# Kernel optimization log

Measured on AMD Instinct MI355X. Metric: run time of the kernel, lower is better.

Reference implementation:

```python
import jax, jax.numpy as jnp
import numpy as np

DIN = 1024
DOUT = 1024
NUM_HEAD = 16
HEAD_DIM = DIN // NUM_HEAD  # 64
SEQ = 2048
BS = 4


def setup_inputs() -> dict:
    key = jax.random.key(0)
    ks = jax.random.split(key, 9)
    s_in = 1.0 / np.sqrt(DIN)
    s_out = 1.0 / np.sqrt(DOUT)
    return {
        "x": jax.random.normal(ks[0], (BS, SEQ, DIN), dtype=jnp.float32),
        "Wq": jax.random.normal(ks[1], (DIN, DOUT), dtype=jnp.float32) * s_in,
        "bq": jax.random.normal(ks[2], (DOUT,), dtype=jnp.float32) * s_in,
        "Wk": jax.random.normal(ks[3], (DIN, DOUT), dtype=jnp.float32) * s_in,
        "bk": jax.random.normal(ks[4], (DOUT,), dtype=jnp.float32) * s_in,
        "Wv": jax.random.normal(ks[5], (DIN, DOUT), dtype=jnp.float32) * s_in,
        "bv": jax.random.normal(ks[6], (DOUT,), dtype=jnp.float32) * s_in,
        "Wo": jax.random.normal(ks[7], (DOUT, DOUT), dtype=jnp.float32) * s_out,
        "bo": jax.random.normal(ks[8], (DOUT,), dtype=jnp.float32) * s_out,
    }


def reference(x, Wq, bq, Wk, bk, Wv, bv, Wo, bo):
    bs, n, _ = x.shape
    # projections -> [bs, n, H, hd] -> [bs, H, n, hd]
    def split_heads(t):
        return t.reshape(bs, n, NUM_HEAD, HEAD_DIM).transpose(0, 2, 1, 3)

    q = split_heads(x @ Wq + bq)
    k = split_heads(x @ Wk + bk)
    v = split_heads(x @ Wv + bv)

    # full [bs, H, n, n] scores, causal mask, scaled softmax
    scores = jnp.einsum("bhqd,bhkd->bhqk", q, k)
    causal = jnp.tril(jnp.ones((n, n), dtype=bool))
    scores = jnp.where(causal, scores, -jnp.inf)
    att = jax.nn.softmax(scores / np.sqrt(HEAD_DIM), axis=-1)

    ctx = jnp.einsum("bhqk,bhkd->bhqd", att, v)
    ctx = ctx.transpose(0, 2, 1, 3).reshape(bs, n, DOUT)
    return ctx @ Wo + bo
```

## Files before the change

kernel.cpp:

```cpp
#include <hip/hip_runtime.h>
#include <hip/hip_bf16.h>
#include <stdint.h>

#define DIN   1024
#define DOUT  1024
#define NHEAD 16
#define HDIM  64
#define SEQL  2048
#define BSZ   4
#define MTOT  (BSZ*SEQL)
#define KDIM  1024

typedef __bf16 bf16x8 __attribute__((ext_vector_type(8)));
typedef float  f32x4  __attribute__((ext_vector_type(4)));

__device__ __forceinline__ f32x4 mfma16(bf16x8 a, bf16x8 b, f32x4 c) {
    return __builtin_amdgcn_mfma_f32_16x16x32_bf16(a, b, c, 0, 0, 0);
}

__device__ __forceinline__ void gl_lds16(const void* gsrc, void* ldst) {
    __builtin_amdgcn_global_load_lds(
        (const __attribute__((address_space(1))) uint32_t*)gsrc,
        (__attribute__((address_space(3))) uint32_t*)ldst, 16, 0, 0);
}

#if __has_builtin(__builtin_amdgcn_exp2f)
__device__ __forceinline__ float fexp2(float x) { return __builtin_amdgcn_exp2f(x); }
#else
__device__ __forceinline__ float fexp2(float x) { return exp2f(x); }
#endif

__device__ __forceinline__ unsigned int cvtpk(float lo, float hi) {
    unsigned int r;
    asm("v_cvt_pk_bf16_f32 %0, %1, %2" : "=v"(r) : "v"(lo), "v"(hi));
    return r;
}

__device__ __forceinline__ unsigned short f2bf(float f) {
    union { __hip_bfloat16 h; unsigned short u; } cv;
    cv.h = __float2bfloat16(f);
    return cv.u;
}

__global__ void cvt_bf16(const float4* __restrict__ in, ushort4* __restrict__ out, int n4) {
    int idx = blockIdx.x * blockDim.x + threadIdx.x;
    int stride = gridDim.x * blockDim.x;
    for (int i = idx; i < n4; i += stride) {
        float4 v = in[i];
        ushort4 o;
        o.x = f2bf(v.x); o.y = f2bf(v.y); o.z = f2bf(v.z); o.w = f2bf(v.w);
        out[i] = o;
    }
}

__global__ void transpose_cvt3(const float* __restrict__ W0, const float* __restrict__ W1,
                               const float* __restrict__ W2, __hip_bfloat16* __restrict__ Wt3) {
    __shared__ __hip_bfloat16 t[32][33];
    const int tx = threadIdx.x, ty = threadIdx.y;
    const int bx = blockIdx.x, by = blockIdx.y, z = blockIdx.z;
    const float* W = (z == 0) ? W0 : (z == 1) ? W1 : W2;
    __hip_bfloat16* Wt = Wt3 + (size_t)z * DOUT * DIN;
#pragma unroll
    for (int r = 0; r < 4; ++r)
        t[ty + 8*r][tx] = __float2bfloat16(W[(size_t)(by*32 + ty + 8*r) * DOUT + bx*32 + tx]);
    __syncthreads();
#pragma unroll
    for (int r = 0; r < 4; ++r)
        Wt[(size_t)(bx*32 + ty + 8*r) * DIN + by*32 + tx] = t[tx][ty + 8*r];
}

__global__ void transpose_cvt(const float* __restrict__ W, __hip_bfloat16* __restrict__ Wt) {
    __shared__ __hip_bfloat16 t[32][33];
    const int tx = threadIdx.x, ty = threadIdx.y;
    const int bx = blockIdx.x, by = blockIdx.y;
#pragma unroll
    for (int r = 0; r < 4; ++r)
        t[ty + 8*r][tx] = __float2bfloat16(W[(size_t)(by*32 + ty + 8*r) * DOUT + bx*32 + tx]);
    __syncthreads();
#pragma unroll
    for (int r = 0; r < 4; ++r)
        Wt[(size_t)(bx*32 + ty + 8*r) * DIN + by*32 + tx] = t[tx][ty + 8*r];
}

template <int EPI>
__global__ __launch_bounds__(256)
void gemm_mfma(const __hip_bfloat16* __restrict__ A,
               const __hip_bfloat16* __restrict__ Bt,
               const float* __restrict__ b0, const float* __restrict__ b1,
               void* __restrict__ o0, void* __restrict__ o1,
               float scale)
{
    __shared__ alignas(16) __hip_bfloat16 As[2][4][128][8];
    __shared__ alignas(16) __hip_bfloat16 Bs[2][4][128][8];

    const int tid  = threadIdx.x;
    const int w    = tid >> 6;
    const int lane = tid & 63;
    const int g    = lane >> 4;
    const int r    = lane & 15;
    const int wr   = w >> 1, wc = w & 1;

    const int row0 = blockIdx.y * 128;
    const int col0 = blockIdx.x * 128;

    f32x4 acc[4][4];
#pragma unroll
    for (int m = 0; m < 4; ++m)
#pragma unroll
        for (int n = 0; n < 4; ++n) acc[m][n] = (f32x4)0.0f;

    auto stage = [&](int buf, int kt) {
        const __hip_bfloat16* ga = A  + (size_t)(row0 + lane) * KDIM + kt*32 + 8*w;
        const __hip_bfloat16* gb = Bt + (size_t)(col0 + lane) * KDIM + kt*32 + 8*w;
        gl_lds16(ga,            &As[buf][w][0][0]);
        gl_lds16(ga + 64*KDIM,  &As[buf][w][64][0]);
        gl_lds16(gb,            &Bs[buf][w][0][0]);
        gl_lds16(gb + 64*KDIM,  &Bs[buf][w][64][0]);
    };

    stage(0, 0);
    __syncthreads();

    const int NKT = KDIM / 32;
    for (int kt = 0; kt < NKT; ++kt) {
        const int cur = kt & 1;
        if (kt + 1 < NKT) stage(cur ^ 1, kt + 1);

        bf16x8 af[4], bfr[4];
#pragma unroll
        for (int m = 0; m < 4; ++m)
            af[m] = *reinterpret_cast<const bf16x8*>(&As[cur][g][64*wr + 16*m + r][0]);
#pragma unroll
        for (int n = 0; n < 4; ++n)
            bfr[n] = *reinterpret_cast<const bf16x8*>(&Bs[cur][g][64*wc + 16*n + r][0]);

#pragma unroll
        for (int m = 0; m < 4; ++m)
#pragma unroll
            for (int n = 0; n < 4; ++n) {
                if (EPI == 1) acc[m][n] = mfma16(af[m], bfr[n], acc[m][n]);
                else          acc[m][n] = mfma16(bfr[n], af[m], acc[m][n]);
            }

        __syncthreads();
    }

    if (EPI == 0) {
        const int slab = col0 >> 10;
        const float* bp = (slab == 0) ? b0 : b1;
        __hip_bfloat16* op = (__hip_bfloat16*)((slab == 0) ? o0 : o1);
        const float sc = (slab == 0) ? scale : 1.0f;
#pragma unroll
        for (int m = 0; m < 4; ++m) {
            const int rowg = row0 + 64*wr + 16*m + r;
            const int bb = rowg >> 11, sq = rowg & (SEQL-1);
#pragma unroll
            for (int n = 0; n < 4; ++n) {
                const int c2 = (col0 & 1023) + 64*wc + 16*n + 4*g;
                const int hh = c2 >> 6, dd = c2 & (HDIM-1);
                const float4 bv4 = *reinterpret_cast<const float4*>(&bp[c2]);
                ushort4 ov;
                ov.x = f2bf((acc[m][n][0] + bv4.x) * sc);
                ov.y = f2bf((acc[m][n][1] + bv4.y) * sc);
                ov.z = f2bf((acc[m][n][2] + bv4.z) * sc);
                ov.w = f2bf((acc[m][n][3] + bv4.w) * sc);
                *reinterpret_cast<ushort4*>(
                    &op[(((size_t)(bb*NHEAD + hh) * SEQL + sq) << 6) + dd]) = ov;
            }
        }
    } else if (EPI == 1) {
#pragma unroll
        for (int n = 0; n < 4; ++n) {
            const int colg = col0 + 64*wc + 16*n + r;
            const int hhd = colg >> 6, dd = colg & (HDIM-1);
            const int n2 = dd >> 4, r2 = dd & 15;
            const float bv_ = b0[colg];
#pragma unroll
            for (int m = 0; m < 4; ++m) {
                const int rowg0 = row0 + 64*wr + 16*m + 4*g;
                const int bb = rowg0 >> 11, sq0 = rowg0 & (SEQL-1);
                const int kb = sq0 >> 6;
                const int hh2 = (sq0 >> 5) & 1;
                const int g2 = (sq0 >> 3) & 3;
                const int e0 = sq0 & 7;
                ushort4 ov;
                ov.x = f2bf(acc[m][n][0] + bv_);
                ov.y = f2bf(acc[m][n][1] + bv_);
                ov.z = f2bf(acc[m][n][2] + bv_);
                ov.w = f2bf(acc[m][n][3] + bv_);
                const size_t off = (size_t)(bb*NHEAD + hhd) * (SEQL*HDIM)
                    + ((((size_t)kb*4 + n2)*2 + hh2)*64 + 16*g2 + r2)*8 + e0;
                *reinterpret_cast<ushort4*>(&((__hip_bfloat16*)o0)[off]) = ov;
            }
        }
    } else {
#pragma unroll
        for (int m = 0; m < 4; ++m) {
            const int rowg = row0 + 64*wr + 16*m + r;
#pragma unroll
            for (int n = 0; n < 4; ++n) {
                const int colg0 = col0 + 64*wc + 16*n + 4*g;
                const float4 bv4 = *reinterpret_cast<const float4*>(&b0[colg0]);
                float4 ov;
                ov.x = acc[m][n][0] + bv4.x;
                ov.y = acc[m][n][1] + bv4.y;
                ov.z = acc[m][n][2] + bv4.z;
                ov.w = acc[m][n][3] + bv4.w;
                *reinterpret_cast<float4*>(&((float*)o0)[(size_t)rowg * DOUT + colg0]) = ov;
            }
        }
    }
}

__global__ __launch_bounds__(256)
void attn_fwd(const __hip_bfloat16* __restrict__ Q,
              const __hip_bfloat16* __restrict__ K,
              const __hip_bfloat16* __restrict__ Vff,
              __hip_bfloat16* __restrict__ ctx)
{
    __shared__ alignas(16) __hip_bfloat16 Ps[4][16][64];
    __shared__ alignas(16) f32x4 Om[2][64][16];
    __shared__ float Ml[2][64][9];

    const int tid  = threadIdx.x;
    const int w    = tid >> 6;
    const int lane = tid & 63;
    const int g    = lane >> 4;
    const int r    = lane & 15;
    const int swz  = (r & 7) << 3;
    const int pp   = w >> 1;
    const int half = w & 1;

    const int bh = blockIdx.x;
    const int b  = bh >> 4, h = bh & 15;

    const __hip_bfloat16* Qh = Q   + (size_t)bh * SEQL * HDIM;
    const __hip_bfloat16* Kh = K   + (size_t)bh * SEQL * HDIM;
    const __hip_bfloat16* Vh = Vff + (size_t)bh * SEQL * HDIM;

    const int sp = blockIdx.y * 2 + pp;

#pragma unroll 1
    for (int ti = 0; ti < 2; ++ti) {
        const int strip = ti ? (31 - sp) : sp;
        const int qb = strip * 64;

        bf16x8 qf[4][2];
#pragma unroll
        for (int m = 0; m < 4; ++m)
#pragma unroll
            for (int hh = 0; hh < 2; ++hh)
                qf[m][hh] = *reinterpret_cast<const bf16x8*>(
                    Qh + (size_t)(qb + 16*m + r) * HDIM + 32*hh + 8*g);

        f32x4 o[4][4];
        float mrow[4], lrow[4];
#pragma unroll
        for (int m = 0; m < 4; ++m) {
#pragma unroll
            for (int n = 0; n < 4; ++n) o[m][n] = (f32x4)0.0f;
            mrow[m] = -1e30f; lrow[m] = 0.0f;
        }

        const int nst = strip + 1;
        const int ns2 = (nst + 1) >> 1;
        const int k0  = half ? ns2 : 0;
        const int k1  = half ? nst : ns2;

        const __hip_bfloat16* kp01 = Kh + (size_t)(k0*64 + r) * HDIM + 8*g;
        const __hip_bfloat16* kp23 = kp01 + 32*HDIM;
        const __hip_bfloat16* vpA = Vh + (size_t)k0 * 4096 + lane * 8;
        const __hip_bfloat16* vpB = vpA + 2048;

#pragma unroll 1
        for (int kt = k0; kt < k1; ++kt) {
            const int key0 = kt * 64;

            bf16x8 kf[4][2], vf[4][2];
#pragma unroll
            for (int hh = 0; hh < 2; ++hh) {
                kf[0][hh] = *reinterpret_cast<const bf16x8*>(kp01 + hh*32);
                kf[1][hh] = *reinterpret_cast<const bf16x8*>(kp01 + 16*HDIM + hh*32);
                kf[2][hh] = *reinterpret_cast<const bf16x8*>(kp23 + hh*32);
                kf[3][hh] = *reinterpret_cast<const bf16x8*>(kp23 + 16*HDIM + hh*32);
                vf[0][hh] = *reinterpret_cast<const bf16x8*>(vpA + hh*512);
                vf[1][hh] = *reinterpret_cast<const bf16x8*>(vpA + 1024 + hh*512);
                vf[2][hh] = *reinterpret_cast<const bf16x8*>(vpB + hh*512);
                vf[3][hh] = *reinterpret_cast<const bf16x8*>(vpB + 1024 + hh*512);
            }
            kp01 += 64*HDIM; kp23 += 64*HDIM;
            vpA += 4096; vpB += 4096;

            const bool lastkt = (kt == nst - 1);

#pragma unroll
            for (int m = 0; m < 4; ++m) {
                f32x4 s[4];
                __builtin_amdgcn_s_setprio(1);
#pragma unroll
                for (int c = 0; c < 4; ++c) {
                    f32x4 t = (f32x4)0.0f;
                    t = mfma16(kf[c][0], qf[m][0], t);
                    t = mfma16(kf[c][1], qf[m][1], t);
                    s[c] = t;
                }
                __builtin_amdgcn_s_setprio(0);

                const int qrow = qb + 16*m + r;
                if (lastkt) {
#pragma unroll
                    for (int c = 0; c < 4; ++c) {
                        const int kb = key0 + 16*c + 4*g;
#pragma unroll
                        for (int j = 0; j < 4; ++j)
                            if (kb + j > qrow) s[c][j] = -1e30f;
                    }
                }

                float t0 = fmaxf(fmaxf(s[0][0], s[0][1]), fmaxf(s[0][2], s[0][3]));
                float t1 = fmaxf(fmaxf(s[1][0], s[1][1]), fmaxf(s[1][2], s[1][3]));
                float t2 = fmaxf(fmaxf(s[2][0], s[2][1]), fmaxf(s[2][2], s[2][3]));
                float t3 = fmaxf(fmaxf(s[3][0], s[3][1]), fmaxf(s[3][2], s[3][3]));
                float pml = fmaxf(fmaxf(t0, t1), fmaxf(t2, t3));

                if (__any(pml > mrow[m] + 11.0f)) {
                    float pm = fmaxf(pml, __shfl_xor(pml, 16));
                    pm = fmaxf(pm, __shfl_xor(pm, 32));
                    const float mnew = fmaxf(mrow[m], pm);
                    const float fac  = fexp2(mrow[m] - mnew);
                    mrow[m] = mnew;
                    lrow[m] *= fac;
#pragma unroll
                    for (int n = 0; n < 4; ++n) o[m][n] *= fac;
                }

                float p[4][4];
#pragma unroll
                for (int c = 0; c < 4; ++c)
#pragma unroll
                    for (int j = 0; j < 4; ++j)
                        p[c][j] = fexp2(s[c][j] - mrow[m]);

                float u0 = (p[0][0] + p[0][1]) + (p[0][2] + p[0][3]);
                float u1 = (p[1][0] + p[1][1]) + (p[1][2] + p[1][3]);
                float u2 = (p[2][0] + p[2][1]) + (p[2][2] + p[2][3]);
                float u3 = (p[3][0] + p[3][1]) + (p[3][2] + p[3][3]);
                lrow[m] += (u0 + u1) + (u2 + u3);

#pragma unroll
                for (int c = 0; c < 4; ++c) {
                    uint2 pk;
                    pk.x = cvtpk(p[c][0], p[c][1]);
                    pk.y = cvtpk(p[c][2], p[c][3]);
                    *reinterpret_cast<uint2*>(&Ps[w][r][(16*c + 4*g) ^ swz]) = pk;
                }

                bf16x8 pf[2];
#pragma unroll
                for (int hh = 0; hh < 2; ++hh)
                    pf[hh] = *reinterpret_cast<const bf16x8*>(
                        &Ps[w][r][(32*hh + 8*g) ^ swz]);

                __builtin_amdgcn_s_setprio(1);
#pragma unroll
                for (int n = 0; n < 4; ++n) {
                    o[m][n] = mfma16(vf[n][0], pf[0], o[m][n]);
                    o[m][n] = mfma16(vf[n][1], pf[1], o[m][n]);
                }
                __builtin_amdgcn_s_setprio(0);
            }
        }

#pragma unroll
        for (int m = 0; m < 4; ++m) {
            lrow[m] += __shfl_xor(lrow[m], 16);
            lrow[m] += __shfl_xor(lrow[m], 32);
        }

        if (half) {
#pragma unroll
            for (int m = 0; m < 4; ++m) {
#pragma unroll
                for (int n = 0; n < 4; ++n)
                    Om[pp][lane][(m*4 + n) ^ (lane & 7)] = o[m][n];
                Ml[pp][lane][m]     = mrow[m];
                Ml[pp][lane][4 + m] = lrow[m];
            }
        }
        __syncthreads();
        if (!half) {
#pragma unroll
            for (int m = 0; m < 4; ++m) {
                const float m1 = Ml[pp][lane][m];
                const float l1 = Ml[pp][lane][4 + m];
                const float M  = fmaxf(mrow[m], m1);
                const float f0 = fexp2(mrow[m] - M);
                const float f1 = fexp2(m1 - M);
                const float L  = lrow[m] * f0 + l1 * f1;
                const float inv = 1.0f / L;
                const size_t rowbase = (size_t)(b*SEQL + qb + 16*m + r) * DOUT + h*HDIM;
#pragma unroll
                for (int n = 0; n < 4; ++n) {
                    const f32x4 o1 = Om[pp][lane][(m*4 + n) ^ (lane & 7)];
                    uint2 ov;
                    ov.x = cvtpk((o[m][n][0]*f0 + o1[0]*f1) * inv,
                                 (o[m][n][1]*f0 + o1[1]*f1) * inv);
                    ov.y = cvtpk((o[m][n][2]*f0 + o1[2]*f1) * inv,
                                 (o[m][n][3]*f0 + o1[3]*f1) * inv);
                    *reinterpret_cast<uint2*>(&ctx[rowbase + 16*n + 4*g]) = ov;
                }
            }
        }
        __syncthreads();
    }
}

extern "C" void kernel_launch(void* const* d_in, const int* in_sizes, int n_in,
                              void* d_out, int out_size, void* d_ws, size_t ws_size,
                              hipStream_t stream) {
    const float* x  = (const float*)d_in[0];
    const float* Wq = (const float*)d_in[1];
    const float* bq = (const float*)d_in[2];
    const float* Wk = (const float*)d_in[3];
    const float* bk = (const float*)d_in[4];
    const float* Wv = (const float*)d_in[5];
    const float* bv = (const float*)d_in[6];
    const float* Wo = (const float*)d_in[7];
    const float* bo = (const float*)d_in[8];
    float* out = (float*)d_out;
    (void)in_sizes; (void)n_in; (void)out_size; (void)ws_size;

    char* ws = (char*)d_ws;
    __hip_bfloat16* xb  = (__hip_bfloat16*)ws;
    __hip_bfloat16* Wt3 = (__hip_bfloat16*)(ws + (16u << 20));
    __hip_bfloat16* Wot = (__hip_bfloat16*)(ws + (22u << 20));
    __hip_bfloat16* Qb  = (__hip_bfloat16*)(ws + (24u << 20));
    __hip_bfloat16* Kb  = Qb + (size_t)MTOT * DOUT;
    __hip_bfloat16* Vtb = Kb + (size_t)MTOT * DOUT;
    __hip_bfloat16* ctx = xb;

    cvt_bf16<<<2048, 256, 0, stream>>>((const float4*)x, (ushort4*)xb, MTOT * DIN / 4);

    dim3 tb(32, 8);
    transpose_cvt3<<<dim3(32, 32, 3), tb, 0, stream>>>(Wq, Wk, Wv, Wt3);
    transpose_cvt <<<dim3(32, 32),    tb, 0, stream>>>(Wo, Wot);

    dim3 gqk(2*DOUT / 128, MTOT / 128);
    gemm_mfma<0><<<gqk, 256, 0, stream>>>(xb, Wt3, bq, bk, Qb, Kb,
                                          0.125f * 1.44269504088896f);
    dim3 gv(DOUT / 128, MTOT / 128);
    gemm_mfma<1><<<gv, 256, 0, stream>>>(xb, Wt3 + (size_t)2*DOUT*DIN, bv, nullptr,
                                         Vtb, nullptr, 1.0f);

    dim3 ag(BSZ * NHEAD, 8);
    attn_fwd<<<ag, 256, 0, stream>>>(Qb, Kb, Vtb, ctx);

    gemm_mfma<2><<<gv, 256, 0, stream>>>(ctx, Wot, bo, nullptr,
                                         out, nullptr, 1.0f);
}
```

Baseline: 260.0 us.

## Enlarge GEMM tile to 256x128 and store K in fragment-friendly layout

```diff
diff --git a/kernel.cpp b/kernel.cpp
--- a/kernel.cpp
+++ b/kernel.cpp
@@ -90,7 +90,7 @@
                void* __restrict__ o0, void* __restrict__ o1,
                float scale)
 {
-    __shared__ alignas(16) __hip_bfloat16 As[2][4][128][8];
+    __shared__ alignas(16) __hip_bfloat16 As[2][4][256][8];
     __shared__ alignas(16) __hip_bfloat16 Bs[2][4][128][8];
 
     const int tid  = threadIdx.x;
@@ -98,24 +98,25 @@
     const int lane = tid & 63;
     const int g    = lane >> 4;
     const int r    = lane & 15;
-    const int wr   = w >> 1, wc = w & 1;
-
-    const int row0 = blockIdx.y * 128;
+
+    const int row0 = blockIdx.y * 256;
     const int col0 = blockIdx.x * 128;
 
-    f32x4 acc[4][4];
+    f32x4 acc[4][8];
 #pragma unroll
     for (int m = 0; m < 4; ++m)
 #pragma unroll
-        for (int n = 0; n < 4; ++n) acc[m][n] = (f32x4)0.0f;
+        for (int n = 0; n < 8; ++n) acc[m][n] = (f32x4)0.0f;
 
     auto stage = [&](int buf, int kt) {
         const __hip_bfloat16* ga = A  + (size_t)(row0 + lane) * KDIM + kt*32 + 8*w;
         const __hip_bfloat16* gb = Bt + (size_t)(col0 + lane) * KDIM + kt*32 + 8*w;
-        gl_lds16(ga,            &As[buf][w][0][0]);
-        gl_lds16(ga + 64*KDIM,  &As[buf][w][64][0]);
-        gl_lds16(gb,            &Bs[buf][w][0][0]);
-        gl_lds16(gb + 64*KDIM,  &Bs[buf][w][64][0]);
+        gl_lds16(ga,             &As[buf][w][0][0]);
+        gl_lds16(ga + 64*KDIM,   &As[buf][w][64][0]);
+        gl_lds16(ga + 128*KDIM,  &As[buf][w][128][0]);
+        gl_lds16(ga + 192*KDIM,  &As[buf][w][192][0]);
+        gl_lds16(gb,             &Bs[buf][w][0][0]);
+        gl_lds16(gb + 64*KDIM,   &Bs[buf][w][64][0]);
     };
 
     stage(0, 0);
@@ -126,18 +127,18 @@
         const int cur = kt & 1;
         if (kt + 1 < NKT) stage(cur ^ 1, kt + 1);
 
-        bf16x8 af[4], bfr[4];
+        bf16x8 af[4], bfr[8];
 #pragma unroll
         for (int m = 0; m < 4; ++m)
-            af[m] = *reinterpret_cast<const bf16x8*>(&As[cur][g][64*wr + 16*m + r][0]);
-#pragma unroll
-        for (int n = 0; n < 4; ++n)
-            bfr[n] = *reinterpret_cast<const bf16x8*>(&Bs[cur][g][64*wc + 16*n + r][0]);
+            af[m] = *reinterpret_cast<const bf16x8*>(&As[cur][g][64*w + 16*m + r][0]);
+#pragma unroll
+        for (int n = 0; n < 8; ++n)
+            bfr[n] = *reinterpret_cast<const bf16x8*>(&Bs[cur][g][16*n + r][0]);
 
 #pragma unroll
         for (int m = 0; m < 4; ++m)
 #pragma unroll
-            for (int n = 0; n < 4; ++n) {
+            for (int n = 0; n < 8; ++n) {
                 if (EPI == 1) acc[m][n] = mfma16(af[m], bfr[n], acc[m][n]);
                 else          acc[m][n] = mfma16(bfr[n], af[m], acc[m][n]);
             }
@@ -147,37 +148,58 @@
 
     if (EPI == 0) {
         const int slab = col0 >> 10;
-        const float* bp = (slab == 0) ? b0 : b1;
-        __hip_bfloat16* op = (__hip_bfloat16*)((slab == 0) ? o0 : o1);
-        const float sc = (slab == 0) ? scale : 1.0f;
-#pragma unroll
-        for (int m = 0; m < 4; ++m) {
-            const int rowg = row0 + 64*wr + 16*m + r;
-            const int bb = rowg >> 11, sq = rowg & (SEQL-1);
-#pragma unroll
-            for (int n = 0; n < 4; ++n) {
-                const int c2 = (col0 & 1023) + 64*wc + 16*n + 4*g;
-                const int hh = c2 >> 6, dd = c2 & (HDIM-1);
-                const float4 bv4 = *reinterpret_cast<const float4*>(&bp[c2]);
-                ushort4 ov;
-                ov.x = f2bf((acc[m][n][0] + bv4.x) * sc);
-                ov.y = f2bf((acc[m][n][1] + bv4.y) * sc);
-                ov.z = f2bf((acc[m][n][2] + bv4.z) * sc);
-                ov.w = f2bf((acc[m][n][3] + bv4.w) * sc);
-                *reinterpret_cast<ushort4*>(
-                    &op[(((size_t)(bb*NHEAD + hh) * SEQL + sq) << 6) + dd]) = ov;
+        if (slab == 0) {
+#pragma unroll
+            for (int m = 0; m < 4; ++m) {
+                const int rowg = row0 + 64*w + 16*m + r;
+                const int bb = rowg >> 11, sq = rowg & (SEQL-1);
+#pragma unroll
+                for (int n = 0; n < 8; ++n) {
+                    const int c2 = (col0 & 1023) + 16*n + 4*g;
+                    const int hd = c2 >> 6, dd = c2 & (HDIM-1);
+                    const float4 bv4 = *reinterpret_cast<const float4*>(&b0[c2]);
+                    ushort4 ov;
+                    ov.x = f2bf((acc[m][n][0] + bv4.x) * scale);
+                    ov.y = f2bf((acc[m][n][1] + bv4.y) * scale);
+                    ov.z = f2bf((acc[m][n][2] + bv4.z) * scale);
+                    ov.w = f2bf((acc[m][n][3] + bv4.w) * scale);
+                    *reinterpret_cast<ushort4*>(
+                        &((__hip_bfloat16*)o0)[(((size_t)(bb*NHEAD + hd) * SEQL + sq) << 6) + dd]) = ov;
+                }
+            }
+        } else {
+#pragma unroll
+            for (int m = 0; m < 4; ++m) {
+                const int rowg = row0 + 64*w + 16*m + r;
+                const int bb = rowg >> 11, sq = rowg & (SEQL-1);
+                const int kb = sq >> 6, cc = (sq >> 4) & 3, r2 = sq & 15;
+#pragma unroll
+                for (int n = 0; n < 8; ++n) {
+                    const int c2 = (col0 & 1023) + 16*n + 4*g;
+                    const int hd = c2 >> 6, dd = c2 & (HDIM-1);
+                    const int hh2 = dd >> 5, g2 = (dd >> 3) & 3, e0 = dd & 7;
+                    const float4 bv4 = *reinterpret_cast<const float4*>(&b1[c2]);
+                    ushort4 ov;
+                    ov.x = f2bf(acc[m][n][0] + bv4.x);
+                    ov.y = f2bf(acc[m][n][1] + bv4.y);
+                    ov.z = f2bf(acc[m][n][2] + bv4.z);
+                    ov.w = f2bf(acc[m][n][3] + bv4.w);
+                    const size_t off = (size_t)(bb*NHEAD + hd) * (SEQL*HDIM)
+                        + ((((size_t)kb*4 + cc)*2 + hh2)*64 + g2*16 + r2)*8 + e0;
+                    *reinterpret_cast<ushort4*>(&((__hip_bfloat16*)o1)[off]) = ov;
+                }
             }
         }
     } else if (EPI == 1) {
 #pragma unroll
-        for (int n = 0; n < 4; ++n) {
-            const int colg = col0 + 64*wc + 16*n + r;
-            const int hhd = colg >> 6, dd = colg & (HDIM-1);
+        for (int n = 0; n < 8; ++n) {
+            const int colg = col0 + 16*n + r;
+            const int hd = colg >> 6, dd = colg & (HDIM-1);
             const int n2 = dd >> 4, r2 = dd & 15;
             const float bv_ = b0[colg];
 #pragma unroll
             for (int m = 0; m < 4; ++m) {
-                const int rowg0 = row0 + 64*wr + 16*m + 4*g;
+                const int rowg0 = row0 + 64*w + 16*m + 4*g;
                 const int bb = rowg0 >> 11, sq0 = rowg0 & (SEQL-1);
                 const int kb = sq0 >> 6;
                 const int hh2 = (sq0 >> 5) & 1;
@@ -188,7 +210,7 @@
                 ov.y = f2bf(acc[m][n][1] + bv_);
                 ov.z = f2bf(acc[m][n][2] + bv_);
                 ov.w = f2bf(acc[m][n][3] + bv_);
-                const size_t off = (size_t)(bb*NHEAD + hhd) * (SEQL*HDIM)
+                const size_t off = (size_t)(bb*NHEAD + hd) * (SEQL*HDIM)
                     + ((((size_t)kb*4 + n2)*2 + hh2)*64 + 16*g2 + r2)*8 + e0;
                 *reinterpret_cast<ushort4*>(&((__hip_bfloat16*)o0)[off]) = ov;
             }
@@ -196,10 +218,10 @@
     } else {
 #pragma unroll
         for (int m = 0; m < 4; ++m) {
-            const int rowg = row0 + 64*wr + 16*m + r;
-#pragma unroll
-            for (int n = 0; n < 4; ++n) {
-                const int colg0 = col0 + 64*wc + 16*n + 4*g;
+            const int rowg = row0 + 64*w + 16*m + r;
+#pragma unroll
+            for (int n = 0; n < 8; ++n) {
+                const int colg0 = col0 + 16*n + 4*g;
                 const float4 bv4 = *reinterpret_cast<const float4*>(&b0[colg0]);
                 float4 ov;
                 ov.x = acc[m][n][0] + bv4.x;
@@ -214,7 +236,7 @@
 
 __global__ __launch_bounds__(256)
 void attn_fwd(const __hip_bfloat16* __restrict__ Q,
-              const __hip_bfloat16* __restrict__ K,
+              const __hip_bfloat16* __restrict__ Kff,
               const __hip_bfloat16* __restrict__ Vff,
               __hip_bfloat16* __restrict__ ctx)
 {
@@ -235,7 +257,7 @@
     const int b  = bh >> 4, h = bh & 15;
 
     const __hip_bfloat16* Qh = Q   + (size_t)bh * SEQL * HDIM;
-    const __hip_bfloat16* Kh = K   + (size_t)bh * SEQL * HDIM;
+    const __hip_bfloat16* Kh = Kff + (size_t)bh * SEQL * HDIM;
     const __hip_bfloat16* Vh = Vff + (size_t)bh * SEQL * HDIM;
 
     const int sp = blockIdx.y * 2 + pp;
@@ -267,8 +289,8 @@
         const int k0  = half ? ns2 : 0;
         const int k1  = half ? nst : ns2;
 
-        const __hip_bfloat16* kp01 = Kh + (size_t)(k0*64 + r) * HDIM + 8*g;
-        const __hip_bfloat16* kp23 = kp01 + 32*HDIM;
+        const __hip_bfloat16* kpA = Kh + (size_t)k0 * 4096 + lane * 8;
+        const __hip_bfloat16* kpB = kpA + 2048;
         const __hip_bfloat16* vpA = Vh + (size_t)k0 * 4096 + lane * 8;
         const __hip_bfloat16* vpB = vpA + 2048;
 
@@ -279,16 +301,16 @@
             bf16x8 kf[4][2], vf[4][2];
 #pragma unroll
             for (int hh = 0; hh < 2; ++hh) {
-                kf[0][hh] = *reinterpret_cast<const bf16x8*>(kp01 + hh*32);
-                kf[1][hh] = *reinterpret_cast<const bf16x8*>(kp01 + 16*HDIM + hh*32);
-                kf[2][hh] = *reinterpret_cast<const bf16x8*>(kp23 + hh*32);
-                kf[3][hh] = *reinterpret_cast<const bf16x8*>(kp23 + 16*HDIM + hh*32);
+                kf[0][hh] = *reinterpret_cast<const bf16x8*>(kpA + hh*512);
+                kf[1][hh] = *reinterpret_cast<const bf16x8*>(kpA + 1024 + hh*512);
+                kf[2][hh] = *reinterpret_cast<const bf16x8*>(kpB + hh*512);
+                kf[3][hh] = *reinterpret_cast<const bf16x8*>(kpB + 1024 + hh*512);
                 vf[0][hh] = *reinterpret_cast<const bf16x8*>(vpA + hh*512);
                 vf[1][hh] = *reinterpret_cast<const bf16x8*>(vpA + 1024 + hh*512);
                 vf[2][hh] = *reinterpret_cast<const bf16x8*>(vpB + hh*512);
                 vf[3][hh] = *reinterpret_cast<const bf16x8*>(vpB + 1024 + hh*512);
             }
-            kp01 += 64*HDIM; kp23 += 64*HDIM;
+            kpA += 4096; kpB += 4096;
             vpA += 4096; vpB += 4096;
 
             const bool lastkt = (kt == nst - 1);
@@ -445,10 +467,10 @@
     transpose_cvt3<<<dim3(32, 32, 3), tb, 0, stream>>>(Wq, Wk, Wv, Wt3);
     transpose_cvt <<<dim3(32, 32),    tb, 0, stream>>>(Wo, Wot);
 
-    dim3 gqk(2*DOUT / 128, MTOT / 128);
+    dim3 gqk(2*DOUT / 128, MTOT / 256);
     gemm_mfma<0><<<gqk, 256, 0, stream>>>(xb, Wt3, bq, bk, Qb, Kb,
                                           0.125f * 1.44269504088896f);
-    dim3 gv(DOUT / 128, MTOT / 128);
+    dim3 gv(DOUT / 128, MTOT / 256);
     gemm_mfma<1><<<gv, 256, 0, stream>>>(xb, Wt3 + (size_t)2*DOUT*DIN, bv, nullptr,
                                          Vtb, nullptr, 1.0f);
 
```

After: 324.8 us. 1.25x slower.
